# Performance work log

Measured on AMD Instinct MI355X. Metric: run time of the kernel, lower is better.

## Reference

```python
import jax, jax.numpy as jnp
import numpy as np

BITS = 32
HDC_DIM = 512
IN_SCALE = 23  # 1 + 2*input_window_size, window=11


def setup_inputs() -> dict:
    key = jax.random.key(0)
    k1, k2, k3, k4 = jax.random.split(key, 4)
    B = 2
    D = IN_SCALE * IN_SCALE  # 529
    num_nonzero = int(0.5 * D * HDC_DIM)  # 135424
    return {
        "data_input": jax.random.normal(k1, (B, 4 * IN_SCALE, IN_SCALE), dtype=jnp.float32),
        "structure_input": jax.random.normal(k2, (B, IN_SCALE, IN_SCALE), dtype=jnp.float32),
        "parameters_temp": jax.random.uniform(k3, (IN_SCALE, IN_SCALE), dtype=jnp.float32),
        "non_zero_indices": jax.random.randint(k4, (num_nonzero,), 0, D * HDC_DIM, dtype=jnp.int32),
    }


def _bit_unpack(x_float):
    # view float32 bits as int32, unpack into 0/1 per bit (little-endian bit order),
    # matching torch: x.unsqueeze(-1).bitwise_and(2**arange(bits)).ne(0)
    xi = jax.lax.bitcast_convert_type(x_float, jnp.int32)
    mask = jnp.left_shift(jnp.int32(1), jnp.arange(BITS, dtype=jnp.int32))  # [32], incl. sign bit
    return ((xi[..., None] & mask) != 0).astype(jnp.int32)  # [..., 32]


def reference(data_input, structure_input, parameters_temp, non_zero_indices):
    B = data_input.shape[0]
    n = IN_SCALE
    # channel slices
    r = data_input[:, 0:n, :].reshape(B, -1)            # [B, D]
    g = data_input[:, n:2 * n, :].reshape(B, -1)
    b = data_input[:, 2 * n:3 * n, :].reshape(B, -1)
    a = data_input[:, 3 * n:4 * n, :].reshape(B, -1)
    s = (structure_input * parameters_temp).reshape(B, -1)  # [B, D]
    D = r.shape[1]

    # sparse random scatter into flat projection buffer (faithful to torch semantics:
    # view(-1)[idx] = 1, then view(-1)[~idx] = 0 where ~idx indexes total-1-idx via negative wrap)
    total = B * D * BITS * HDC_DIM
    proj = jnp.zeros((total,), dtype=jnp.int32)
    proj = proj.at[non_zero_indices].set(1)
    proj = proj.at[total - 1 - non_zero_indices].set(0)
    proj = proj.reshape(B, D, BITS, HDC_DIM)

    # bit-unpack + broadcast-XOR against projection (no materialized repeat)
    r_bin = _bit_unpack(r)[..., None] ^ proj  # [B, D, 32, hdc]
    g_bin = _bit_unpack(g)[..., None] ^ proj
    b_bin = _bit_unpack(b)[..., None] ^ proj
    a_bin = _bit_unpack(a)[..., None] ^ proj
    s_bin = _bit_unpack(s)[..., None] ^ proj

    return (r, g, b, a, s, r_bin, g_bin, b_bin, a_bin, s_bin)
```

## Files before the change

kernel.cpp:

```cpp
#include <hip/hip_runtime.h>
#include <stdint.h>

#define IN_SCALE 23
#define DDIM 529
#define BATCH 2
#define BITS 32
#define HDC 512
#define NNZ_REGION (DDIM * HDC)
#define SMALL (5 * BATCH * DDIM)
#define BIN_PER_OUT (BATCH * DDIM * BITS * HDC)
#define BIN_PER_B   (DDIM * BITS * HDC)

__global__ void scatter_mask(const int* __restrict__ idx, int n,
                             uint8_t* __restrict__ mask) {
    int i = blockIdx.x * blockDim.x + threadIdx.x;
    if (i < n) {
        int p = idx[i];
        if (p >= 0 && p < NNZ_REGION) mask[p] = 1;
    }
}

__global__ void small_outputs(const float* __restrict__ data,
                              const float* __restrict__ structure,
                              const float* __restrict__ params,
                              float* __restrict__ out,
                              int* __restrict__ xw) {
    int i = blockIdx.x * blockDim.x + threadIdx.x;
    if (i >= SMALL) return;
    int c   = i / (BATCH * DDIM);
    int rem = i % (BATCH * DDIM);
    int bb  = rem / DDIM;
    int d   = rem % DDIM;
    float v;
    if (c < 4) {
        v = data[bb * (4 * DDIM) + c * DDIM + d];
    } else {
        v = structure[bb * DDIM + d] * params[d];
    }
    out[i] = v;
    xw[i] = __float_as_int(v);
}

__global__ __launch_bounds__(256) void bins_kernel(const int* __restrict__ xw,
                                                   const uint8_t* __restrict__ mask,
                                                   float* __restrict__ out) {
    int blk = blockIdx.x;
    int c   = blk / (BATCH * DDIM);
    int rem = blk % (BATCH * DDIM);
    int bb  = rem / DDIM;
    int d   = rem % DDIM;
    int x   = xw[blk];

    long long base_elem = (long long)SMALL + (long long)c * BIN_PER_OUT
                        + (long long)bb * BIN_PER_B
                        + (long long)d * (BITS * HDC);
    float2* o = (float2*)out + (base_elem >> 1);

    int t = threadIdx.x;
    const int dbase = d * (BITS * HDC);
    #pragma unroll
    for (int j = 0; j < BITS; ++j) {
        int bv = (x >> j) & 1;
        float f = (float)bv;
        float2 v = make_float2(f, f);
        int p = dbase + j * HDC + t * 2;
        if (bb == 0 && p < NNZ_REGION) {
            v.x = (float)(bv ^ (int)mask[p]);
            v.y = (float)(bv ^ (int)mask[p + 1]);
        }
        o[j * 256 + t] = v;
    }
}

extern "C" void kernel_launch(void* const* d_in, const int* in_sizes, int n_in,
                              void* d_out, int out_size, void* d_ws, size_t ws_size,
                              hipStream_t stream) {
    const float* data      = (const float*)d_in[0];
    const float* structure = (const float*)d_in[1];
    const float* params    = (const float*)d_in[2];
    const int*   nzi       = (const int*)d_in[3];
    int nnz = in_sizes[3];

    float*   out  = (float*)d_out;
    uint8_t* mask = (uint8_t*)d_ws;
    int*     xw   = (int*)((char*)d_ws + NNZ_REGION);

    hipMemsetAsync(mask, 0, NNZ_REGION, stream);
    scatter_mask<<<(nnz + 255) / 256, 256, 0, stream>>>(nzi, nnz, mask);
    small_outputs<<<(SMALL + 255) / 256, 256, 0, stream>>>(data, structure, params, out, xw);
    bins_kernel<<<SMALL, 256, 0, stream>>>(xw, mask, out);
}
```

Measured before the change: 87.04 us.

## Fuse small-output kernel into bins kernel and write 16-byte aligned float4 stores

```diff
diff --git a/kernel.cpp b/kernel.cpp
--- a/kernel.cpp
+++ b/kernel.cpp
@@ -6,42 +6,24 @@
 #define BATCH 2
 #define BITS 32
 #define HDC 512
+#define ROW (BITS * HDC)
 #define NNZ_REGION (DDIM * HDC)
 #define SMALL (5 * BATCH * DDIM)
-#define BIN_PER_OUT (BATCH * DDIM * BITS * HDC)
-#define BIN_PER_B   (DDIM * BITS * HDC)
+#define BIN_PER_OUT (BATCH * DDIM * ROW)
+#define BIN_PER_B   (DDIM * ROW)
 
 __global__ void scatter_mask(const int* __restrict__ idx, int n,
                              uint8_t* __restrict__ mask) {
     int i = blockIdx.x * blockDim.x + threadIdx.x;
     if (i < n) {
         int p = idx[i];
-        if (p >= 0 && p < NNZ_REGION) mask[p] = 1;
+        if ((unsigned)p < NNZ_REGION) mask[p] = 1;
     }
 }
 
-__global__ void small_outputs(const float* __restrict__ data,
-                              const float* __restrict__ structure,
-                              const float* __restrict__ params,
-                              float* __restrict__ out,
-                              int* __restrict__ xw) {
-    int i = blockIdx.x * blockDim.x + threadIdx.x;
-    if (i >= SMALL) return;
-    int c   = i / (BATCH * DDIM);
-    int rem = i % (BATCH * DDIM);
-    int bb  = rem / DDIM;
-    int d   = rem % DDIM;
-    float v;
-    if (c < 4) {
-        v = data[bb * (4 * DDIM) + c * DDIM + d];
-    } else {
-        v = structure[bb * DDIM + d] * params[d];
-    }
-    out[i] = v;
-    xw[i] = __float_as_int(v);
-}
-
-__global__ __launch_bounds__(256) void bins_kernel(const int* __restrict__ xw,
+__global__ __launch_bounds__(256) void bins_kernel(const float* __restrict__ data,
+                                                   const float* __restrict__ structure,
+                                                   const float* __restrict__ params,
                                                    const uint8_t* __restrict__ mask,
                                                    float* __restrict__ out) {
     int blk = blockIdx.x;
@@ -49,26 +31,52 @@
     int rem = blk % (BATCH * DDIM);
     int bb  = rem / DDIM;
     int d   = rem % DDIM;
-    int x   = xw[blk];
 
-    long long base_elem = (long long)SMALL + (long long)c * BIN_PER_OUT
-                        + (long long)bb * BIN_PER_B
-                        + (long long)d * (BITS * HDC);
-    float2* o = (float2*)out + (base_elem >> 1);
+    float v;
+    if (c < 4) {
+        v = data[bb * (4 * DDIM) + c * DDIM + d];
+    } else {
+        v = structure[bb * DDIM + d] * params[d];
+    }
+    const int x = __float_as_int(v);
+
+    const bool useMask = (bb == 0);
+    const int  dbase   = d * ROW;
+    long long base = (long long)SMALL + (long long)c * BIN_PER_OUT
+                   + (long long)bb * BIN_PER_B + (long long)d * ROW;
+    float* o = out + base;
 
     int t = threadIdx.x;
-    const int dbase = d * (BITS * HDC);
+    if (t == 0) {
+        out[blk] = v;
+        int b0 = x & 1, v0 = b0, v1 = b0;
+        if (useMask && dbase < NNZ_REGION) { v0 ^= mask[dbase]; v1 ^= mask[dbase + 1]; }
+        *(float2*)o = make_float2((float)v0, (float)v1);
+    } else if (t == 1) {
+        int b31 = (x >> 31) & 1, v0 = b31, v1 = b31;
+        int p = dbase + ROW - 2;
+        if (useMask && p < NNZ_REGION) { v0 ^= mask[p]; v1 ^= mask[p + 1]; }
+        *(float2*)(o + ROW - 2) = make_float2((float)v0, (float)v1);
+    }
+
+    float4* om = (float4*)(o + 2);
     #pragma unroll
-    for (int j = 0; j < BITS; ++j) {
-        int bv = (x >> j) & 1;
-        float f = (float)bv;
-        float2 v = make_float2(f, f);
-        int p = dbase + j * HDC + t * 2;
-        if (bb == 0 && p < NNZ_REGION) {
-            v.x = (float)(bv ^ (int)mask[p]);
-            v.y = (float)(bv ^ (int)mask[p + 1]);
+    for (int k = 0; k < 16; ++k) {
+        int q = t + k * 256;
+        if (q < 4095) {
+            int e0 = 2 + q * 4;
+            float4 w;
+            float* wp = (float*)&w;
+            #pragma unroll
+            for (int u = 0; u < 4; ++u) {
+                int e  = e0 + u;
+                int bv = (x >> (e >> 9)) & 1;
+                int p  = dbase + e;
+                if (useMask && p < NNZ_REGION) bv ^= mask[p];
+                wp[u] = (float)bv;
+            }
+            om[q] = w;
         }
-        o[j * 256 + t] = v;
     }
 }
 
@@ -83,10 +91,8 @@
 
     float*   out  = (float*)d_out;
     uint8_t* mask = (uint8_t*)d_ws;
-    int*     xw   = (int*)((char*)d_ws + NNZ_REGION);
 
     hipMemsetAsync(mask, 0, NNZ_REGION, stream);
     scatter_mask<<<(nnz + 255) / 256, 256, 0, stream>>>(nzi, nnz, mask);
-    small_outputs<<<(SMALL + 255) / 256, 256, 0, stream>>>(data, structure, params, out, xw);
-    bins_kernel<<<SMALL, 256, 0, stream>>>(xw, mask, out);
+    bins_kernel<<<SMALL, 256, 0, stream>>>(data, structure, params, mask, out);
 }
```

Result: no change. 86.10 us (-1.1%).
